# Kernel tuning notes

Hardware: AMD Instinct MI355X
Metric: run time of the kernel (lower is better)

## Reference

```python
import jax, jax.numpy as jnp
import numpy as np


def _topk_gate(v, k):
    # keep values >= k-th largest (ties kept, matching torch semantics)
    topk_vals = jax.lax.top_k(v, k)[0]          # (B, k)
    thr = topk_vals[:, -1:]                      # (B, 1)
    return v * (v >= thr).astype(v.dtype)


def setup_inputs() -> dict:
    key = jax.random.key(0)
    ks = jax.random.split(key, 12)
    B, S, D, R, M = 8, 2048, 1024, 64, 256
    H = 4 * D
    def lin(k, fan_out, fan_in):
        bound = 1.0 / np.sqrt(fan_in)
        return jax.random.uniform(k, (fan_out, fan_in), jnp.float32, -bound, bound)
    def bias(k, fan_out, fan_in):
        bound = 1.0 / np.sqrt(fan_in)
        return jax.random.uniform(k, (fan_out,), jnp.float32, -bound, bound)
    return {
        "x": jax.random.normal(ks[0], (B, S, D), jnp.float32),
        "state": jnp.zeros((B, M), jnp.float32),
        "U_w": lin(ks[1], R, D),
        "V_w": lin(ks[2], R, D),
        "w1": lin(ks[3], H, D),
        "b1": bias(ks[4], H, D),
        "w2": lin(ks[5], D, H),
        "b2": bias(ks[6], D, H),
        "win_w": lin(ks[7], M, D),
        "win_b": bias(ks[8], M, D),
        "wstate": lin(ks[9], M, M),
        "gamma": jnp.float32(0.9),
        "top_k": 32,
    }


def reference(x, state, U_w, V_w, w1, b1, w2, b2, win_w, win_b, wstate, gamma, top_k):
    # outputs depend only on x (residual + FFN), computed vectorized over seq.
    h = jax.nn.relu(jnp.einsum("bsd,hd->bsh", x, w1) + b1)
    outputs = x + jnp.einsum("bsh,dh->bsd", h, w2) + b2   # (B, S, D)
    # Note: U_proj / V_proj are computed but unused in the original forward
    # (dead code); omitted here as they do not affect outputs or memory.

    # precompute W_in projection for all timesteps: (B, S, M)
    x_proj = jnp.einsum("bsd,md->bsm", x, win_w) + win_b

    def step(carry, xp_t):
        st, mem = carry
        su = jax.nn.relu(st @ wstate.T + xp_t)            # (B, M)
        g = _topk_gate(su, top_k)
        mem = gamma * mem + (1.0 - gamma) * g
        return (g, mem), None

    (_, memory), _ = jax.lax.scan(step, (state, state), jnp.swapaxes(x_proj, 0, 1))
    return outputs, memory
```

## Files before the change

### kernel.cpp

```cpp
#include <hip/hip_runtime.h>
#include <stdint.h>

#define BB 8
#define SS 2048
#define DD 1024
#define HH 4096
#define MM 256
#define NWORK 248

typedef short bf16x8 __attribute__((ext_vector_type(8)));
typedef float f32x4 __attribute__((ext_vector_type(4)));

__device__ inline unsigned short f2bf(float f){
  unsigned u = __builtin_bit_cast(unsigned, f);
  return (unsigned short)((u + 0x7FFFu + ((u >> 16) & 1u)) >> 16);
}

__global__ void ssma_pack_bf16(const float* __restrict__ src,
                               unsigned short* __restrict__ dst, int n4){
  int i = blockIdx.x * blockDim.x + threadIdx.x;
  if (i < n4){
    float4 v = ((const float4*)src)[i];
    ushort4 o;
    o.x = f2bf(v.x); o.y = f2bf(v.y); o.z = f2bf(v.z); o.w = f2bf(v.w);
    ((ushort4*)dst)[i] = o;
  }
}

__global__ __launch_bounds__(256) void ssma_gemm3_f32(
    const float* __restrict__ A, const float* __restrict__ Bw,
    const float* __restrict__ bias, float* __restrict__ C)
{
  __shared__ float As[64][17];
  __shared__ float Bs[64][17];
  const int tid = threadIdx.x;
  const int tx = tid & 15, ty = tid >> 4;
  const int m0 = blockIdx.y * 64, n0 = blockIdx.x * 64;
  float acc[4][4];
#pragma unroll
  for (int i = 0; i < 4; ++i)
#pragma unroll
    for (int j = 0; j < 4; ++j) acc[i][j] = 0.f;

  for (int k0 = 0; k0 < DD; k0 += 16){
    __syncthreads();
#pragma unroll
    for (int i = 0; i < 4; ++i){
      int e = tid + 256 * i;
      int r = e >> 4, c = e & 15;
      As[r][c] = A [(size_t)(m0 + r) * DD + k0 + c];
      Bs[r][c] = Bw[(size_t)(n0 + r) * DD + k0 + c];
    }
    __syncthreads();
#pragma unroll
    for (int kk = 0; kk < 16; ++kk){
      float a[4], b[4];
#pragma unroll
      for (int i = 0; i < 4; ++i) a[i] = As[ty * 4 + i][kk];
#pragma unroll
      for (int j = 0; j < 4; ++j) b[j] = Bs[tx * 4 + j][kk];
#pragma unroll
      for (int i = 0; i < 4; ++i)
#pragma unroll
        for (int j = 0; j < 4; ++j) acc[i][j] = fmaf(a[i], b[j], acc[i][j]);
    }
  }
#pragma unroll
  for (int i = 0; i < 4; ++i){
    int row = m0 + ty * 4 + i;
#pragma unroll
    for (int j = 0; j < 4; ++j){
      int col = n0 + tx * 4 + j;
      C[(size_t)row * MM + col] = acc[i][j] + bias[col];
    }
  }
}

__global__ __launch_bounds__(256) void ssma_transpose(
    const float* __restrict__ A, float* __restrict__ At)
{
  __shared__ float t[32][33];
  const int tx = threadIdx.x & 31, ty = threadIdx.x >> 5;
  const int x0 = blockIdx.x * 32, y0 = blockIdx.y * 32;
#pragma unroll
  for (int r = 0; r < 32; r += 8)
    t[ty + r][tx] = A[(size_t)(y0 + ty + r) * MM + x0 + tx];
  __syncthreads();
#pragma unroll
  for (int r = 0; r < 32; r += 8)
    At[(size_t)(x0 + ty + r) * MM + y0 + tx] = t[tx][ty + r];
}

template<int EPI>
__device__ void gemm_tile(const unsigned short* __restrict__ A,
                          const unsigned short* __restrict__ Bw,
                          int K, int N, const float* __restrict__ bias,
                          const float* __restrict__ resid, void* __restrict__ Cout,
                          int bx, int by, uint4* As4, uint4* Bs4)
{
  const int tid  = threadIdx.x;
  const int lane = tid & 63;
  const int wv   = tid >> 6;
  const int wm   = wv >> 1, wn = wv & 1;
  const int m0   = by * 128;
  const int n0   = bx * 128;
  const int kq   = lane >> 4;
  const int rl   = lane & 15;

  f32x4 acc[4][4];
#pragma unroll
  for (int a = 0; a < 4; ++a)
#pragma unroll
    for (int b = 0; b < 4; ++b) acc[a][b] = (f32x4){0.f, 0.f, 0.f, 0.f};

  for (int k0 = 0; k0 < K; k0 += 32){
    __syncthreads();
#pragma unroll
    for (int i = 0; i < 2; ++i){
      int c  = tid + 256 * i;
      int r  = c >> 2;
      int c8 = (c & 3) * 8;
      As4[c] = *(const uint4*)(A  + (size_t)(m0 + r) * K + k0 + c8);
      Bs4[c] = *(const uint4*)(Bw + (size_t)(n0 + r) * K + k0 + c8);
    }
    __syncthreads();

    const bf16x8* Ap = (const bf16x8*)As4;
    const bf16x8* Bp = (const bf16x8*)Bs4;
    bf16x8 af[4], bfr[4];
#pragma unroll
    for (int mi = 0; mi < 4; ++mi) af[mi]  = Ap[(wm * 64 + mi * 16 + rl) * 4 + kq];
#pragma unroll
    for (int ni = 0; ni < 4; ++ni) bfr[ni] = Bp[(wn * 64 + ni * 16 + rl) * 4 + kq];
#pragma unroll
    for (int mi = 0; mi < 4; ++mi)
#pragma unroll
      for (int ni = 0; ni < 4; ++ni)
        acc[mi][ni] = __builtin_amdgcn_mfma_f32_16x16x32_bf16(af[mi], bfr[ni], acc[mi][ni], 0, 0, 0);
  }

#pragma unroll
  for (int mi = 0; mi < 4; ++mi){
#pragma unroll
    for (int ni = 0; ni < 4; ++ni){
      int col = n0 + wn * 64 + ni * 16 + rl;
      float bv = bias[col];
#pragma unroll
      for (int r = 0; r < 4; ++r){
        int row = m0 + wm * 64 + mi * 16 + kq * 4 + r;
        float v = acc[mi][ni][r] + bv;
        if (EPI == 0){
          v = fmaxf(v, 0.0f);
          ((unsigned short*)Cout)[(size_t)row * N + col] = f2bf(v);
        } else {
          v += resid[(size_t)row * N + col];
          ((float*)Cout)[(size_t)row * N + col] = v;
        }
      }
    }
  }
}

__global__ __launch_bounds__(256, 1) void ssma_fused3(
    const float* __restrict__ xproj, const float* __restrict__ state,
    const float* __restrict__ wT, const float* __restrict__ gamma_p,
    const int* __restrict__ topk_p, float* __restrict__ mem_out,
    const unsigned short* __restrict__ xb, const unsigned short* __restrict__ w1b,
    const unsigned short* __restrict__ w2b, unsigned short* __restrict__ hbuf,
    const float* __restrict__ b1, const float* __restrict__ b2,
    const float* __restrict__ xres, float* __restrict__ out,
    unsigned int* __restrict__ ctr)
{
  extern __shared__ char dynpad[];
  __shared__ uint4 As4[512];
  __shared__ uint4 Bs4[512];
  __shared__ __align__(16) float su_all[MM];
  __shared__ __align__(16) int   hist[256];
  __shared__ __align__(16) int   kidx[MM + 32];
  __shared__ __align__(16) float kval[MM + 32];
  __shared__ __align__(16) unsigned long long umask[4];
  __shared__ __align__(16) unsigned long long bmask[4];
  (void)dynpad;

  const int tid = threadIdx.x;

  if (blockIdx.x >= 8){
    const int wid = blockIdx.x - 8;
    for (int t = wid; t < 4096; t += NWORK)
      gemm_tile<0>(xb, w1b, 1024, 4096, b1, nullptr, (void*)hbuf, t & 31, t >> 5, As4, Bs4);
    __syncthreads();
    if (tid == 0){
      __threadfence();
      atomicAdd(ctr, 1u);
      while (__hip_atomic_load(ctr, __ATOMIC_RELAXED, __HIP_MEMORY_SCOPE_AGENT) < NWORK)
        __builtin_amdgcn_s_sleep(16);
    }
    __syncthreads();
    __threadfence();
    for (int t = wid; t < 1024; t += NWORK)
      gemm_tile<1>(hbuf, w2b, 4096, 1024, b2, xres, (void*)out, t & 7, t >> 3, As4, Bs4);
    return;
  }

  const int b    = blockIdx.x;
  const int wv   = tid >> 6;
  const int lane = tid & 63;
  const float gamma = *gamma_p;
  const float omg   = 1.0f - gamma;
  const int   K     = *topk_p;

  const float* xp  = xproj + (size_t)b * SS * MM;
  const float* wTm = wT + tid;

  if (tid < 64) ((int4*)hist)[tid] = (int4){0, 0, 0, 0};

  float mem = state[b * MM + tid];
  float st0 = mem;
  {
    unsigned long long pmi = __ballot(st0 != 0.0f);
    if (lane == 0) umask[wv] = pmi;
  }
  __syncthreads();
  int nkp;
  {
    unsigned long long u0 = umask[0], u1 = umask[1], u2 = umask[2], u3 = umask[3];
    int nk = __popcll(u0) + __popcll(u1) + __popcll(u2) + __popcll(u3);
    if (st0 != 0.0f){
      int before = (wv > 0 ? __popcll(u0) : 0) + (wv > 1 ? __popcll(u1) : 0)
                 + (wv > 2 ? __popcll(u2) : 0);
      unsigned long long mw = (wv == 0 ? u0 : wv == 1 ? u1 : wv == 2 ? u2 : u3);
      int pos = before + __popcll(mw & ((1ull << lane) - 1ull));
      kidx[pos] = tid << 8;
      kval[pos] = st0;
    }
    nkp = (nk + 3) & ~3; if (nkp < 32) nkp = 32;
    if (tid < 64 && nk + tid < nkp){ kidx[nk + tid] = 0; kval[nk + tid] = 0.0f; }
  }
  float xp_cur = xp[tid];
  __syncthreads();

  for (int t = 0; t < SS; ++t){
    int tn = (t + 1 < SS) ? t + 1 : SS - 1;
    float xp_next = xp[(size_t)tn * MM + tid];

    const int4*   ip = (const int4*)kidx;
    const float4* vp = (const float4*)kval;
    int4   I[8];
    float4 V[8];
#pragma unroll
    for (int j = 0; j < 8; ++j){ I[j] = ip[j]; V[j] = vp[j]; }
    float a0=0.f,a1=0.f,a2=0.f,a3=0.f,a4=0.f,a5=0.f,a6=0.f,a7=0.f;
    float w00=wTm[I[0].x], w01=wTm[I[0].y], w02=wTm[I[0].z], w03=wTm[I[0].w];
    float w10=wTm[I[1].x], w11=wTm[I[1].y], w12=wTm[I[1].z], w13=wTm[I[1].w];
    float w20=wTm[I[2].x], w21=wTm[I[2].y], w22=wTm[I[2].z], w23=wTm[I[2].w];
    float w30=wTm[I[3].x], w31=wTm[I[3].y], w32=wTm[I[3].z], w33=wTm[I[3].w];
    float w40=wTm[I[4].x], w41=wTm[I[4].y], w42=wTm[I[4].z], w43=wTm[I[4].w];
    float w50=wTm[I[5].x], w51=wTm[I[5].y], w52=wTm[I[5].z], w53=wTm[I[5].w];
    float w60=wTm[I[6].x], w61=wTm[I[6].y], w62=wTm[I[6].z], w63=wTm[I[6].w];
    float w70=wTm[I[7].x], w71=wTm[I[7].y], w72=wTm[I[7].z], w73=wTm[I[7].w];
    a0=fmaf(w00,V[0].x,a0); a0=fmaf(w01,V[0].y,a0); a0=fmaf(w02,V[0].z,a0); a0=fmaf(w03,V[0].w,a0);
    a1=fmaf(w10,V[1].x,a1); a1=fmaf(w11,V[1].y,a1); a1=fmaf(w12,V[1].z,a1); a1=fmaf(w13,V[1].w,a1);
    a2=fmaf(w20,V[2].x,a2); a2=fmaf(w21,V[2].y,a2); a2=fmaf(w22,V[2].z,a2); a2=fmaf(w23,V[2].w,a2);
    a3=fmaf(w30,V[3].x,a3); a3=fmaf(w31,V[3].y,a3); a3=fmaf(w32,V[3].z,a3); a3=fmaf(w33,V[3].w,a3);
    a4=fmaf(w40,V[4].x,a4); a4=fmaf(w41,V[4].y,a4); a4=fmaf(w42,V[4].z,a4); a4=fmaf(w43,V[4].w,a4);
    a5=fmaf(w50,V[5].x,a5); a5=fmaf(w51,V[5].y,a5); a5=fmaf(w52,V[5].z,a5); a5=fmaf(w53,V[5].w,a5);
    a6=fmaf(w60,V[6].x,a6); a6=fmaf(w61,V[6].y,a6); a6=fmaf(w62,V[6].z,a6); a6=fmaf(w63,V[6].w,a6);
    a7=fmaf(w70,V[7].x,a7); a7=fmaf(w71,V[7].y,a7); a7=fmaf(w72,V[7].z,a7); a7=fmaf(w73,V[7].w,a7);
    if (nkp > 32){
      for (int c4 = 8; c4 < (nkp >> 2); ++c4){
        int4 I2 = ip[c4]; float4 V2 = vp[c4];
        a0 = fmaf(wTm[I2.x], V2.x, a0); a1 = fmaf(wTm[I2.y], V2.y, a1);
        a2 = fmaf(wTm[I2.z], V2.z, a2); a3 = fmaf(wTm[I2.w], V2.w, a3);
      }
    }
    float s = ((a0 + a1) + (a2 + a3)) + ((a4 + a5) + (a6 + a7));
    float su = fmaxf(s + xp_cur, 0.0f);
    su_all[tid] = su;

    int bin = 0;
    if (su > 0.0f){
      int key = (int)(__float_as_uint(su) >> 21) - 0x160;
      bin = key < 0 ? 0 : (key > 255 ? 255 : key);
      atomicAdd(&hist[bin], 1);
    }
    __syncthreads();

    int4 h4 = ((const int4*)hist)[lane];
    int t4 = h4.x + h4.y + h4.z + h4.w;
    int inc = t4;
#pragma unroll
    for (int off = 1; off < 64; off <<= 1){
      int xv = __shfl_down(inc, off);
      inc += (lane + off < 64) ? xv : 0;
    }
    int E = inc - t4;
    int4 s4;
    s4.w = E;
    s4.z = E + h4.w;
    s4.y = s4.z + h4.z;
    s4.x = s4.y + h4.y;

    int addr = (bin >> 2) << 2;
    int gx = __builtin_amdgcn_ds_bpermute(addr, s4.x);
    int gy = __builtin_amdgcn_ds_bpermute(addr, s4.y);
    int gz = __builtin_amdgcn_ds_bpermute(addr, s4.z);
    int gw = __builtin_amdgcn_ds_bpermute(addr, s4.w);
    int bq = bin & 3;
    int a  = bq == 0 ? gx : bq == 1 ? gy : bq == 2 ? gz : gw;
    int hb = hist[bin];

    float g = 0.0f;
    bool bnd = false;
    if (su > 0.0f){
      if (a >= K)            g = 0.0f;
      else if (a + hb <= K)  g = su;
      else                   bnd = true;
    }
    {
      unsigned long long bm = __ballot(bnd);
      if (lane == 0) bmask[wv] = bm;
    }
    __syncthreads();

    if (bnd){
      int w = 0;
#pragma unroll
      for (int w4 = 0; w4 < 4; ++w4){
        unsigned long long u = bmask[w4];
        while (u){
          int j = __ffsll((long long)u) - 1;
          u &= u - 1;
          w += (su_all[w4 * 64 + j] > su);
        }
      }
      g = (a + w <= K - 1) ? su : 0.0f;
    }
    mem = fmaf(gamma, mem, omg * g);
    {
      unsigned long long pm = __ballot(g > 0.0f);
      if (lane == 0) umask[wv] = pm;
    }
    __syncthreads();

    {
      unsigned long long u0 = umask[0], u1 = umask[1], u2 = umask[2], u3 = umask[3];
      int nk = __popcll(u0) + __popcll(u1) + __popcll(u2) + __popcll(u3);
      if (g > 0.0f){
        int before = (wv > 0 ? __popcll(u0) : 0) + (wv > 1 ? __popcll(u1) : 0)
                   + (wv > 2 ? __popcll(u2) : 0);
        unsigned long long mw = (wv == 0 ? u0 : wv == 1 ? u1 : wv == 2 ? u2 : u3);
        int pos = before + __popcll(mw & ((1ull << lane) - 1ull));
        kidx[pos] = tid << 8;
        kval[pos] = g;
      }
      nkp = (nk + 3) & ~3; if (nkp < 32) nkp = 32;
      if (tid < 64 && nk + tid < nkp){ kidx[nk + tid] = 0; kval[nk + tid] = 0.0f; }
      if (tid >= 64 && tid < 128) ((int4*)hist)[tid - 64] = (int4){0, 0, 0, 0};
    }
    xp_cur = xp_next;
    __syncthreads();
  }
  mem_out[b * MM + tid] = mem;
}

extern "C" void kernel_launch(void* const* d_in, const int* in_sizes, int n_in,
                              void* d_out, int out_size, void* d_ws, size_t ws_size,
                              hipStream_t stream)
{
  const float* x      = (const float*)d_in[0];
  const float* state  = (const float*)d_in[1];
  const float* w1     = (const float*)d_in[4];
  const float* b1     = (const float*)d_in[5];
  const float* w2     = (const float*)d_in[6];
  const float* b2     = (const float*)d_in[7];
  const float* win_w  = (const float*)d_in[8];
  const float* win_b  = (const float*)d_in[9];
  const float* wstate = (const float*)d_in[10];
  const float* gammap = (const float*)d_in[11];
  const int*   topkp  = (const int*)d_in[12];

  float* out  = (float*)d_out;
  float* memo = out + (size_t)BB * SS * DD;

  char* ws = (char*)d_ws;
  unsigned short* xb   = (unsigned short*)(ws);
  unsigned short* w1b  = (unsigned short*)(ws + 33554432);
  unsigned short* w2b  = (unsigned short*)(ws + 41943040);
  unsigned short* hbuf = (unsigned short*)(ws + 50331648);
  float*          xprj = (float*)(ws + 184549376);
  float*          wT   = (float*)(ws + 201326592);
  unsigned int*   ctr  = (unsigned int*)(ws + 201326592 + 262144);

  ssma_pack_bf16<<<16384, 256, 0, stream>>>(x,  xb,  4194304);
  ssma_pack_bf16<<<4096,  256, 0, stream>>>(w1, w1b, 1048576);
  ssma_pack_bf16<<<4096,  256, 0, stream>>>(w2, w2b, 1048576);

  ssma_gemm3_f32<<<dim3(4, 256), 256, 0, stream>>>(x, win_w, win_b, xprj);
  ssma_transpose<<<dim3(8, 8), 256, 0, stream>>>(wstate, wT);

  hipMemsetAsync(ctr, 0, 8, stream);

  ssma_fused3<<<8 + NWORK, 256, 90112, stream>>>(
      xprj, state, wT, gammap, topkp, memo,
      xb, w1b, w2b, hbuf, b1, b2, x, out, ctr);
}
```

Measured before the change: 4.850 ms.

## Fold prep kernels into persistent megakernel and bucket top-k boundary resolution

Moves the bf16 packing, x·W_in projection GEMM and wstate transpose into the worker blocks of one persistent kernel, using a second grid-wide atomic counter so the 8 recurrence blocks wait on the first phase. This removes five separate launches and their serialization. In the scan loop, each histogram bin now stores up to 12 values, so ties at the top-k boundary are resolved per bin without an extra ballot and barrier. Plain barriers are replaced by an lgkm-wait barrier. The trade-off is that the recurrence now waits for the packing and projection work, and the dynamic shared-memory padding that limited occupancy is removed.

Result: slower. 12.61 ms (+159.9%).

```diff
diff --git a/kernel.cpp b/kernel.cpp
--- a/kernel.cpp
+++ b/kernel.cpp
@@ -7,6 +7,7 @@
 #define HH 4096
 #define MM 256
 #define NWORK 248
+#define BKT 12
 
 typedef short bf16x8 __attribute__((ext_vector_type(8)));
 typedef float f32x4 __attribute__((ext_vector_type(4)));
@@ -16,10 +17,20 @@
   return (unsigned short)((u + 0x7FFFu + ((u >> 16) & 1u)) >> 16);
 }
 
-__global__ void ssma_pack_bf16(const float* __restrict__ src,
-                               unsigned short* __restrict__ dst, int n4){
-  int i = blockIdx.x * blockDim.x + threadIdx.x;
-  if (i < n4){
+__device__ inline int su_bin(float v){
+  int key = (int)(__float_as_uint(v) >> 21) - 0x160;
+  return key < 0 ? 0 : (key > 255 ? 255 : key);
+}
+
+__device__ inline void bar_lgkm(){
+  __builtin_amdgcn_sched_barrier(0);
+  asm volatile("s_waitcnt lgkmcnt(0)\n\ts_barrier" ::: "memory");
+  __builtin_amdgcn_sched_barrier(0);
+}
+
+__device__ void d_pack(const float* __restrict__ src, unsigned short* __restrict__ dst,
+                       int n4, int gi, int stride){
+  for (int i = gi; i < n4; i += stride){
     float4 v = ((const float4*)src)[i];
     ushort4 o;
     o.x = f2bf(v.x); o.y = f2bf(v.y); o.z = f2bf(v.z); o.w = f2bf(v.w);
@@ -27,15 +38,13 @@
   }
 }
 
-__global__ __launch_bounds__(256) void ssma_gemm3_f32(
-    const float* __restrict__ A, const float* __restrict__ Bw,
-    const float* __restrict__ bias, float* __restrict__ C)
+__device__ void gemm3_tile(const float* __restrict__ A, const float* __restrict__ Bw,
+                           const float* __restrict__ bias, float* __restrict__ C,
+                           int bx, int by, float (*As)[17], float (*Bs)[17])
 {
-  __shared__ float As[64][17];
-  __shared__ float Bs[64][17];
   const int tid = threadIdx.x;
   const int tx = tid & 15, ty = tid >> 4;
-  const int m0 = blockIdx.y * 64, n0 = blockIdx.x * 64;
+  const int m0 = by * 64, n0 = bx * 64;
   float acc[4][4];
 #pragma unroll
   for (int i = 0; i < 4; ++i)
@@ -65,6 +74,7 @@
         for (int j = 0; j < 4; ++j) acc[i][j] = fmaf(a[i], b[j], acc[i][j]);
     }
   }
+  __syncthreads();
 #pragma unroll
   for (int i = 0; i < 4; ++i){
     int row = m0 + ty * 4 + i;
@@ -76,12 +86,12 @@
   }
 }
 
-__global__ __launch_bounds__(256) void ssma_transpose(
-    const float* __restrict__ A, float* __restrict__ At)
+__device__ void transpose_tile(const float* __restrict__ A, float* __restrict__ At,
+                               int bx, int by, float (*t)[33])
 {
-  __shared__ float t[32][33];
   const int tx = threadIdx.x & 31, ty = threadIdx.x >> 5;
-  const int x0 = blockIdx.x * 32, y0 = blockIdx.y * 32;
+  const int x0 = bx * 32, y0 = by * 32;
+  __syncthreads();
 #pragma unroll
   for (int r = 0; r < 32; r += 8)
     t[ty + r][tx] = A[(size_t)(y0 + ty + r) * MM + x0 + tx];
@@ -89,6 +99,7 @@
 #pragma unroll
   for (int r = 0; r < 32; r += 8)
     At[(size_t)(x0 + ty + r) * MM + y0 + tx] = t[tx][ty + r];
+  __syncthreads();
 }
 
 template<int EPI>
@@ -161,44 +172,66 @@
   }
 }
 
-__global__ __launch_bounds__(256, 1) void ssma_fused3(
-    const float* __restrict__ xproj, const float* __restrict__ state,
-    const float* __restrict__ wT, const float* __restrict__ gamma_p,
-    const int* __restrict__ topk_p, float* __restrict__ mem_out,
-    const unsigned short* __restrict__ xb, const unsigned short* __restrict__ w1b,
-    const unsigned short* __restrict__ w2b, unsigned short* __restrict__ hbuf,
-    const float* __restrict__ b1, const float* __restrict__ b2,
-    const float* __restrict__ xres, float* __restrict__ out,
+__global__ __launch_bounds__(256, 1) void ssma_mega(
+    const float* __restrict__ x, const float* __restrict__ state,
+    const float* __restrict__ w1, const float* __restrict__ b1,
+    const float* __restrict__ w2, const float* __restrict__ b2,
+    const float* __restrict__ win_w, const float* __restrict__ win_b,
+    const float* __restrict__ wstate, const float* __restrict__ gamma_p,
+    const int* __restrict__ topk_p,
+    unsigned short* __restrict__ xb, unsigned short* __restrict__ w1b,
+    unsigned short* __restrict__ w2b, unsigned short* __restrict__ hbuf,
+    float* __restrict__ xprj, float* __restrict__ wT,
+    float* __restrict__ out, float* __restrict__ memo,
     unsigned int* __restrict__ ctr)
 {
-  extern __shared__ char dynpad[];
   __shared__ uint4 As4[512];
   __shared__ uint4 Bs4[512];
+  __shared__ float g3As[64][17];
+  __shared__ float g3Bs[64][17];
   __shared__ __align__(16) float su_all[MM];
   __shared__ __align__(16) int   hist[256];
+  __shared__ __align__(16) float bval[256 * BKT];
   __shared__ __align__(16) int   kidx[MM + 32];
   __shared__ __align__(16) float kval[MM + 32];
   __shared__ __align__(16) unsigned long long umask[4];
-  __shared__ __align__(16) unsigned long long bmask[4];
-  (void)dynpad;
 
   const int tid = threadIdx.x;
 
   if (blockIdx.x >= 8){
     const int wid = blockIdx.x - 8;
+    const int gi = wid * 256 + tid, stride = NWORK * 256;
+
+    d_pack(x,  xb,  4194304, gi, stride);
+    d_pack(w1, w1b, 1048576, gi, stride);
+    d_pack(w2, w2b, 1048576, gi, stride);
+    for (int t = wid; t < 1024; t += NWORK)
+      gemm3_tile(x, win_w, win_b, xprj, t & 3, t >> 2, g3As, g3Bs);
+    for (int t = wid; t < 64; t += NWORK)
+      transpose_tile(wstate, wT, t & 7, t >> 3, (float(*)[33])&g3As[0][0]);
+    __syncthreads();
+    if (tid == 0){
+      __threadfence();
+      atomicAdd(&ctr[0], 1u);
+      while (__hip_atomic_load(&ctr[0], __ATOMIC_RELAXED, __HIP_MEMORY_SCOPE_AGENT) < NWORK)
+        __builtin_amdgcn_s_sleep(8);
+    }
+    __syncthreads();
+    __threadfence();
+
     for (int t = wid; t < 4096; t += NWORK)
       gemm_tile<0>(xb, w1b, 1024, 4096, b1, nullptr, (void*)hbuf, t & 31, t >> 5, As4, Bs4);
     __syncthreads();
     if (tid == 0){
       __threadfence();
-      atomicAdd(ctr, 1u);
-      while (__hip_atomic_load(ctr, __ATOMIC_RELAXED, __HIP_MEMORY_SCOPE_AGENT) < NWORK)
-        __builtin_amdgcn_s_sleep(16);
+      atomicAdd(&ctr[1], 1u);
+      while (__hip_atomic_load(&ctr[1], __ATOMIC_RELAXED, __HIP_MEMORY_SCOPE_AGENT) < NWORK)
+        __builtin_amdgcn_s_sleep(8);
     }
     __syncthreads();
     __threadfence();
     for (int t = wid; t < 1024; t += NWORK)
-      gemm_tile<1>(hbuf, w2b, 4096, 1024, b2, xres, (void*)out, t & 7, t >> 3, As4, Bs4);
+      gemm_tile<1>(hbuf, w2b, 4096, 1024, b2, x, (void*)out, t & 7, t >> 3, As4, Bs4);
     return;
   }
 
@@ -209,7 +242,14 @@
   const float omg   = 1.0f - gamma;
   const int   K     = *topk_p;
 
-  const float* xp  = xproj + (size_t)b * SS * MM;
+  if (tid == 0){
+    while (__hip_atomic_load(&ctr[0], __ATOMIC_ACQUIRE, __HIP_MEMORY_SCOPE_AGENT) < NWORK)
+      __builtin_amdgcn_s_sleep(8);
+  }
+  __syncthreads();
+  __threadfence();
+
+  const float* xp  = xprj + (size_t)b * SS * MM;
   const float* wTm = wT + tid;
 
   if (tid < 64) ((int4*)hist)[tid] = (int4){0, 0, 0, 0};
@@ -279,11 +319,11 @@
 
     int bin = 0;
     if (su > 0.0f){
-      int key = (int)(__float_as_uint(su) >> 21) - 0x160;
-      bin = key < 0 ? 0 : (key > 255 ? 255 : key);
-      atomicAdd(&hist[bin], 1);
-    }
-    __syncthreads();
+      bin = su_bin(su);
+      int slot = atomicAdd(&hist[bin], 1);
+      if (slot < BKT) bval[bin * BKT + slot] = su;
+    }
+    bar_lgkm();
 
     int4 h4 = ((const int4*)hist)[lane];
     int t4 = h4.x + h4.y + h4.z + h4.w;
@@ -310,37 +350,28 @@
     int hb = hist[bin];
 
     float g = 0.0f;
-    bool bnd = false;
     if (su > 0.0f){
       if (a >= K)            g = 0.0f;
       else if (a + hb <= K)  g = su;
-      else                   bnd = true;
-    }
-    {
-      unsigned long long bm = __ballot(bnd);
-      if (lane == 0) bmask[wv] = bm;
-    }
-    __syncthreads();
-
-    if (bnd){
-      int w = 0;
-#pragma unroll
-      for (int w4 = 0; w4 < 4; ++w4){
-        unsigned long long u = bmask[w4];
-        while (u){
-          int j = __ffsll((long long)u) - 1;
-          u &= u - 1;
-          w += (su_all[w4 * 64 + j] > su);
+      else {
+        int w = 0;
+        if (hb <= BKT){
+          for (int j = 0; j < hb; ++j) w += (bval[bin * BKT + j] > su);
+        } else {
+          for (int j = 0; j < MM; ++j){
+            float v = su_all[j];
+            w += (v > su) && (su_bin(v) == bin);
+          }
         }
+        g = (a + w <= K - 1) ? su : 0.0f;
       }
-      g = (a + w <= K - 1) ? su : 0.0f;
     }
     mem = fmaf(gamma, mem, omg * g);
     {
       unsigned long long pm = __ballot(g > 0.0f);
       if (lane == 0) umask[wv] = pm;
     }
-    __syncthreads();
+    bar_lgkm();
 
     {
       unsigned long long u0 = umask[0], u1 = umask[1], u2 = umask[2], u3 = umask[3];
@@ -358,9 +389,9 @@
       if (tid >= 64 && tid < 128) ((int4*)hist)[tid - 64] = (int4){0, 0, 0, 0};
     }
     xp_cur = xp_next;
-    __syncthreads();
-  }
-  mem_out[b * MM + tid] = mem;
+    bar_lgkm();
+  }
+  memo[b * MM + tid] = mem;
 }
 
 extern "C" void kernel_launch(void* const* d_in, const int* in_sizes, int n_in,
@@ -391,16 +422,9 @@
   float*          wT   = (float*)(ws + 201326592);
   unsigned int*   ctr  = (unsigned int*)(ws + 201326592 + 262144);
 
-  ssma_pack_bf16<<<16384, 256, 0, stream>>>(x,  xb,  4194304);
-  ssma_pack_bf16<<<4096,  256, 0, stream>>>(w1, w1b, 1048576);
-  ssma_pack_bf16<<<4096,  256, 0, stream>>>(w2, w2b, 1048576);
-
-  ssma_gemm3_f32<<<dim3(4, 256), 256, 0, stream>>>(x, win_w, win_b, xprj);
-  ssma_transpose<<<dim3(8, 8), 256, 0, stream>>>(wstate, wT);
-
   hipMemsetAsync(ctr, 0, 8, stream);
 
-  ssma_fused3<<<8 + NWORK, 256, 90112, stream>>>(
-      xprj, state, wT, gammap, topkp, memo,
-      xb, w1b, w2b, hbuf, b1, b2, x, out, ctr);
-}
+  ssma_mega<<<8 + NWORK, 256, 0, stream>>>(
+      x, state, w1, b1, w2, b2, win_w, win_b, wstate, gammap, topkp,
+      xb, w1b, w2b, hbuf, xprj, wT, out, memo, ctr);
+}
```
